# Kernel optimization log

Hardware: AMD Instinct MI355X
Metric: run time of the kernel (lower is better)

## Reference

```python
import jax, jax.numpy as jnp
import numpy as np
import math

D_MODEL = 640
HEAD_DIM = 64
N_HEADS = 14
N_KV_HEADS = 2
HPK = N_HEADS // N_KV_HEADS  # 7
EPS = 1e-5
T = 2048
D_HALF = HEAD_DIM // 2


def setup_inputs() -> dict:
    key = jax.random.key(0)
    ks = jax.random.split(key, 10)
    x = jax.random.normal(ks[0], (1, D_MODEL, 1, T), dtype=jnp.float32)
    # rope tables: realistic cos/sin from standard rotary frequencies
    inv_freq = 1.0 / (10000.0 ** (jnp.arange(0, HEAD_DIM, 2, dtype=jnp.float32) / HEAD_DIM))
    ang = jnp.arange(T, dtype=jnp.float32)[:, None] * inv_freq[None, :]  # (T, 32)
    rope_cos = jnp.cos(ang)
    rope_sin = jnp.sin(ang)
    # causal additive mask (T, T)
    causal = jnp.tril(jnp.ones((T, T), dtype=bool))
    attn_mask = jnp.where(causal, 0.0, -1e9).astype(jnp.float32)
    norm_w = 1.0 + 0.02 * jax.random.normal(ks[1], (D_MODEL,), dtype=jnp.float32)
    qkv_dim = (N_HEADS + 2 * N_KV_HEADS) * HEAD_DIM  # 1152
    qkv_w = jax.random.normal(ks[2], (qkv_dim, D_MODEL), dtype=jnp.float32) * (D_MODEL ** -0.5)
    qkv_b = 0.02 * jax.random.normal(ks[3], (qkv_dim,), dtype=jnp.float32)
    o_w = jax.random.normal(ks[4], (D_MODEL, N_HEADS * HEAD_DIM), dtype=jnp.float32) * ((N_HEADS * HEAD_DIM) ** -0.5)
    o_b = 0.02 * jax.random.normal(ks[5], (D_MODEL,), dtype=jnp.float32)
    sinks = jax.random.normal(ks[6], (N_HEADS,), dtype=jnp.float32)
    return {"x": x, "rope_cos": rope_cos, "rope_sin": rope_sin, "attn_mask": attn_mask,
            "norm_w": norm_w, "qkv_w": qkv_w, "qkv_b": qkv_b, "o_w": o_w, "o_b": o_b,
            "sinks": sinks}


def _apply_rope(xf, n_heads, rope_cos, rope_sin):
    # xf: (1, T, n_heads*dh) -> interleaved rotary
    xr = xf.reshape(1, T, n_heads, HEAD_DIM)
    x1 = xr[..., 0::2]  # (1, T, n, d_half)
    x2 = xr[..., 1::2]
    cos = rope_cos[None, :, None, :]
    sin = rope_sin[None, :, None, :]
    o1 = x1 * cos - x2 * sin
    o2 = x2 * cos + x1 * sin
    return jnp.stack((o1, o2), axis=-1).reshape(1, T, n_heads * HEAD_DIM)


def reference(x, rope_cos, rope_sin, attn_mask, norm_w, qkv_w, qkv_b, o_w, o_b, sinks):
    nh, nkv, hpk, dh = N_HEADS, N_KV_HEADS, HPK, HEAD_DIM
    residual = x
    # RMSNorm over channel dim (axis=1)
    var = jnp.mean(x * x, axis=1, keepdims=True)
    normed = x * jax.lax.rsqrt(var + EPS) * norm_w.reshape(1, -1, 1, 1)
    # fused 1x1 conv QKV: (1, D, T) -> (1, T, qkv_dim)
    n2 = normed[:, :, 0, :]  # (1, D, T)
    qkv = jnp.einsum('bct,oc->bto', n2, qkv_w) + qkv_b
    q_dim = nh * dh
    kv_dim = nkv * dh
    q = qkv[:, :, :q_dim]
    k = qkv[:, :, q_dim:q_dim + kv_dim]
    v = qkv[:, :, q_dim + kv_dim:]
    q = _apply_rope(q, nh, rope_cos, rope_sin)
    k = _apply_rope(k, nkv, rope_cos, rope_sin)
    qk_scale = 1.0 / math.sqrt(math.sqrt(dh))
    q = q * qk_scale
    k = k * qk_scale
    q = q.reshape(1, T, nkv, hpk, dh)
    k = k.reshape(1, T, nkv, dh)
    v = v.reshape(1, T, nkv, dh)
    # GQA scores: (1, nkv, hpk, T, T)
    scores = jnp.einsum('btkgd,bskd->bkgts', q, k)
    scores = scores + attn_mask[None, None, None, :, :]
    # attention-sink logit column appended before softmax
    sink = (sinks * math.log(2.0)).reshape(1, nkv, hpk, 1, 1)
    sink_col = jnp.broadcast_to(sink, (1, nkv, hpk, T, 1))
    scores_with_sink = jnp.concatenate([scores, sink_col], axis=-1)
    attn_w = jax.nn.softmax(scores_with_sink, axis=-1)[..., :-1]
    # weighted values: (1, T, nkv, hpk, dh) -> (1, T, nh*dh)
    attn_out = jnp.einsum('bkgts,bskd->btkgd', attn_w, v).reshape(1, T, nh * dh)
    # output 1x1 conv + residual
    proj = jnp.einsum('bto,do->bdt', attn_out, o_w) + o_b.reshape(1, -1, 1)
    return residual + proj[:, :, None, :]
```

## Files before the change

### kernel.cpp

```cpp
#include <hip/hip_runtime.h>
#include <math.h>

#define T 2048
#define DM 640
#define NH 14
#define NKV 2
#define HPK 7
#define HD 64
#define QDIM 896
#define QKV_DIM 1152

constexpr float QK_SCALE2 = 0.35355339059327373f * 1.2011224087864498f;
constexpr float EPSF = 1e-5f;

typedef __attribute__((ext_vector_type(8))) short short8;
typedef __attribute__((ext_vector_type(4))) float float4v;
typedef unsigned short ush;

static __device__ __forceinline__ ush f2bf(float f) {
    union { float f; unsigned u; } v; v.f = f;
    unsigned r = v.u + 0x7fffu + ((v.u >> 16) & 1u);
    return (ush)(r >> 16);
}
static __device__ __forceinline__ float bf2f(ush s) {
    union { unsigned u; float f; } v; v.u = ((unsigned)s) << 16;
    return v.f;
}

__global__ __launch_bounds__(256) void rstd_kernel(
    const float* __restrict__ x, float* __restrict__ rstd)
{
    const int t0 = blockIdx.x * 64;
    const int tl = threadIdx.x & 63, cg = threadIdx.x >> 6;
    __shared__ float red[4][64];
    float ss = 0.f;
    for (int c = cg; c < DM; c += 4) {
        const float v = x[(size_t)c * T + t0 + tl];
        ss = fmaf(v, v, ss);
    }
    red[cg][tl] = ss;
    __syncthreads();
    if (threadIdx.x < 64) {
        const float s = red[0][tl] + red[1][tl] + red[2][tl] + red[3][tl];
        rstd[t0 + tl] = rsqrtf(s * (1.0f / DM) + EPSF);
    }
}

__global__ __launch_bounds__(256) void cast2_kernel(
    const float* __restrict__ a, ush* __restrict__ ah, ush* __restrict__ al, int na4,
    const float* __restrict__ b, ush* __restrict__ bh, ush* __restrict__ bl)
{
    const int i = blockIdx.x * 256 + threadIdx.x;
    const float* src; ush *dh, *dl; int j;
    if (i < na4) { src = a; dh = ah; dl = al; j = i; }
    else         { src = b; dh = bh; dl = bl; j = i - na4; }
    const float4 v = ((const float4*)src)[j];
    ushort4 h, l;
    h.x = f2bf(v.x); l.x = f2bf(v.x - bf2f(h.x));
    h.y = f2bf(v.y); l.y = f2bf(v.y - bf2f(h.y));
    h.z = f2bf(v.z); l.z = f2bf(v.z - bf2f(h.z));
    h.w = f2bf(v.w); l.w = f2bf(v.w - bf2f(h.w));
    ((ushort4*)dh)[j] = h;
    ((ushort4*)dl)[j] = l;
}

__global__ __launch_bounds__(256) void xnorm_kernel(
    const float* __restrict__ x, const float* __restrict__ norm_w,
    const float* __restrict__ rstd,
    ush* __restrict__ XnH, ush* __restrict__ XnL)
{
    const int tid = threadIdx.x;
    const int t0 = blockIdx.x * 64;
    const int c0 = blockIdx.y * 64;
    __shared__ float xs[64][65];

    #pragma unroll
    for (int it = 0; it < 4; ++it) {
        const int r = (tid >> 4) + it * 16;
        const int cl = (tid & 15) * 4;
        const float4 v = *(const float4*)&x[(size_t)(c0 + r) * T + t0 + cl];
        xs[r][cl + 0] = v.x; xs[r][cl + 1] = v.y;
        xs[r][cl + 2] = v.z; xs[r][cl + 3] = v.w;
    }
    __syncthreads();
    #pragma unroll
    for (int it = 0; it < 4; ++it) {
        const int tr = (tid >> 4) + it * 16;
        const int cl = (tid & 15) * 4;
        const float rs = rstd[t0 + tr];
        ushort4 h, l;
        const float v0 = xs[cl + 0][tr] * norm_w[c0 + cl + 0] * rs;
        const float v1 = xs[cl + 1][tr] * norm_w[c0 + cl + 1] * rs;
        const float v2 = xs[cl + 2][tr] * norm_w[c0 + cl + 2] * rs;
        const float v3 = xs[cl + 3][tr] * norm_w[c0 + cl + 3] * rs;
        h.x = f2bf(v0); l.x = f2bf(v0 - bf2f(h.x));
        h.y = f2bf(v1); l.y = f2bf(v1 - bf2f(h.y));
        h.z = f2bf(v2); l.z = f2bf(v2 - bf2f(h.z));
        h.w = f2bf(v3); l.w = f2bf(v3 - bf2f(h.w));
        *(ushort4*)&XnH[(size_t)(t0 + tr) * DM + c0 + cl] = h;
        *(ushort4*)&XnL[(size_t)(t0 + tr) * DM + c0 + cl] = l;
    }
}

#define QSX_H 0
#define QSX_L 8192
#define QSW_H 16384
#define QSW_L 24576

__global__ __launch_bounds__(256) void qkv_mfma_kernel(
    const ush* __restrict__ XnH, const ush* __restrict__ XnL,
    const ush* __restrict__ WH, const ush* __restrict__ WL,
    const float* __restrict__ qkv_b, const float* __restrict__ rope_cos,
    const float* __restrict__ rope_sin,
    ush* __restrict__ Qh, ush* __restrict__ Ql,
    ush* __restrict__ Kh, ush* __restrict__ Kl,
    ush* __restrict__ Vth, ush* __restrict__ Vtl)
{
    const int t0 = blockIdx.x * 64;
    const int o0 = blockIdx.y * 64;
    const int tid = threadIdx.x;
    const int wave = tid >> 6, lane = tid & 63;
    const int lg = lane >> 4, lq = lane & 15;
    const int wr = wave >> 1, wc = wave & 1;

    __shared__ __align__(16) unsigned char sm[65536];

    const int srow0 = tid >> 3, srow1 = srow0 + 32, scc = tid & 7;
    const int dst0 = srow0 * 128 + ((scc * 16) ^ ((srow0 & 7) << 4));
    const int dst1 = srow1 * 128 + ((scc * 16) ^ ((srow1 & 7) << 4));

    uint4 xh0, xl0, wh0, wl0, xh1, xl1, wh1, wl1;

#define QLOAD(c_) do { \
    xh0 = *(const uint4*)&XnH[(size_t)(t0 + srow0) * DM + (c_) + scc * 8]; \
    xl0 = *(const uint4*)&XnL[(size_t)(t0 + srow0) * DM + (c_) + scc * 8]; \
    wh0 = *(const uint4*)&WH [(size_t)(o0 + srow0) * DM + (c_) + scc * 8]; \
    wl0 = *(const uint4*)&WL [(size_t)(o0 + srow0) * DM + (c_) + scc * 8]; \
    xh1 = *(const uint4*)&XnH[(size_t)(t0 + srow1) * DM + (c_) + scc * 8]; \
    xl1 = *(const uint4*)&XnL[(size_t)(t0 + srow1) * DM + (c_) + scc * 8]; \
    wh1 = *(const uint4*)&WH [(size_t)(o0 + srow1) * DM + (c_) + scc * 8]; \
    wl1 = *(const uint4*)&WL [(size_t)(o0 + srow1) * DM + (c_) + scc * 8]; \
} while (0)

#define QSTORE(b_) do { \
    *(uint4*)((b_) + QSX_H + dst0) = xh0; \
    *(uint4*)((b_) + QSX_L + dst0) = xl0; \
    *(uint4*)((b_) + QSW_H + dst0) = wh0; \
    *(uint4*)((b_) + QSW_L + dst0) = wl0; \
    *(uint4*)((b_) + QSX_H + dst1) = xh1; \
    *(uint4*)((b_) + QSX_L + dst1) = xl1; \
    *(uint4*)((b_) + QSW_H + dst1) = wh1; \
    *(uint4*)((b_) + QSW_L + dst1) = wl1; \
} while (0)

    float4v acc[2][2];
    acc[0][0] = (float4v)0.f; acc[0][1] = (float4v)0.f;
    acc[1][0] = (float4v)0.f; acc[1][1] = (float4v)0.f;

    QLOAD(0);
    QSTORE(sm);
    int cur = 0;
    for (int s = 0; s < 10; ++s) {
        __syncthreads();
        if (s < 9) QLOAD((s + 1) * 64);
        const unsigned char* smb = sm + cur * 32768;
        #pragma unroll
        for (int kk = 0; kk < 2; ++kk) {
            short8 ah[2], al[2], bh[2], bl[2];
            #pragma unroll
            for (int nt = 0; nt < 2; ++nt) {
                const int row = wc * 32 + nt * 16 + lq;
                const int col = (kk * 64 + lg * 16) ^ ((row & 7) << 4);
                bh[nt] = *(const short8*)(smb + QSX_H + row * 128 + col);
                bl[nt] = *(const short8*)(smb + QSX_L + row * 128 + col);
            }
            #pragma unroll
            for (int mt = 0; mt < 2; ++mt) {
                const int row = wr * 32 + mt * 16 + lq;
                const int col = (kk * 64 + lg * 16) ^ ((row & 7) << 4);
                ah[mt] = *(const short8*)(smb + QSW_H + row * 128 + col);
                al[mt] = *(const short8*)(smb + QSW_L + row * 128 + col);
            }
            #pragma unroll
            for (int mt = 0; mt < 2; ++mt) {
                #pragma unroll
                for (int nt = 0; nt < 2; ++nt) {
                    acc[mt][nt] = __builtin_amdgcn_mfma_f32_16x16x32_bf16(ah[mt], bh[nt], acc[mt][nt], 0, 0, 0);
                    acc[mt][nt] = __builtin_amdgcn_mfma_f32_16x16x32_bf16(ah[mt], bl[nt], acc[mt][nt], 0, 0, 0);
                    acc[mt][nt] = __builtin_amdgcn_mfma_f32_16x16x32_bf16(al[mt], bh[nt], acc[mt][nt], 0, 0, 0);
                }
            }
        }
        if (s < 9) { QSTORE(sm + ((cur ^ 1) * 32768)); cur ^= 1; }
    }
#undef QLOAD
#undef QSTORE

    const int by = blockIdx.y;
    #pragma unroll
    for (int mt = 0; mt < 2; ++mt) {
        const int d0 = wr * 32 + mt * 16 + lg * 4;
        #pragma unroll
        for (int nt = 0; nt < 2; ++nt) {
            const int t = t0 + wc * 32 + nt * 16 + lq;
            if (by < 16) {
                const float e0 = acc[mt][nt][0] + qkv_b[o0 + d0 + 0];
                const float d1 = acc[mt][nt][1] + qkv_b[o0 + d0 + 1];
                const float e2 = acc[mt][nt][2] + qkv_b[o0 + d0 + 2];
                const float d3 = acc[mt][nt][3] + qkv_b[o0 + d0 + 3];
                const float c0v = rope_cos[t * 32 + (d0 >> 1)];
                const float s0v = rope_sin[t * 32 + (d0 >> 1)];
                const float c1v = rope_cos[t * 32 + (d0 >> 1) + 1];
                const float s1v = rope_sin[t * 32 + (d0 >> 1) + 1];
                const float r0 = (e0 * c0v - d1 * s0v) * QK_SCALE2;
                const float r1 = (d1 * c0v + e0 * s0v) * QK_SCALE2;
                const float r2 = (e2 * c1v - d3 * s1v) * QK_SCALE2;
                const float r3 = (d3 * c1v + e2 * s1v) * QK_SCALE2;
                ushort4 h, l;
                h.x = f2bf(r0); l.x = f2bf(r0 - bf2f(h.x));
                h.y = f2bf(r1); l.y = f2bf(r1 - bf2f(h.y));
                h.z = f2bf(r2); l.z = f2bf(r2 - bf2f(h.z));
                h.w = f2bf(r3); l.w = f2bf(r3 - bf2f(h.w));
                if (by < 14) {
                    *(ushort4*)&Qh[((size_t)(by * T + t)) * HD + d0] = h;
                    *(ushort4*)&Ql[((size_t)(by * T + t)) * HD + d0] = l;
                } else {
                    const int h2 = by - 14;
                    *(ushort4*)&Kh[((size_t)(h2 * T + t)) * HD + d0] = h;
                    *(ushort4*)&Kl[((size_t)(h2 * T + t)) * HD + d0] = l;
                }
            } else {
                const int h2 = by - 16;
                #pragma unroll
                for (int j = 0; j < 4; ++j) {
                    const float val = acc[mt][nt][j] + qkv_b[o0 + d0 + j];
                    const ush hh = f2bf(val);
                    Vth[((size_t)(h2 * HD + d0 + j)) * T + t] = hh;
                    Vtl[((size_t)(h2 * HD + d0 + j)) * T + t] = f2bf(val - bf2f(hh));
                }
            }
        }
    }
}

__global__ __launch_bounds__(256) void attn_mfma_kernel(
    const ush* __restrict__ Qh, const ush* __restrict__ Ql,
    const ush* __restrict__ Kh, const ush* __restrict__ Kl,
    const ush* __restrict__ Vth, const ush* __restrict__ Vtl,
    const float* __restrict__ sinks,
    float* __restrict__ Opart, float* __restrict__ Mpart, float* __restrict__ Lpart)
{
    const int qt = 31 - (int)blockIdx.x;
    const int h  = blockIdx.y;
    const int kc = blockIdx.z;
    const int kvh = h / HPK;
    const int tid = threadIdx.x;
    const int wave = tid >> 6, lane = tid & 63;
    const int lg = lane >> 4, lq = lane & 15;
    const int qbase = qt * 64 + wave * 16;
    const int myq = qbase + lq;

    __shared__ __align__(16) unsigned char sm[2 * 32768 + 4 * 2304];
    unsigned int* Pl = (unsigned int*)(sm + 65536) + wave * (16 * 36);

    short8 qf[2][2];
    #pragma unroll
    for (int kk = 0; kk < 2; ++kk) {
        const size_t qoff = ((size_t)(h * T + myq)) * HD + kk * 32 + lg * 8;
        qf[kk][0] = *(const short8*)&Qh[qoff];
        qf[kk][1] = *(const short8*)&Ql[qoff];
    }

    float4v oacc[4];
    #pragma unroll
    for (int dt = 0; dt < 4; ++dt) oacc[dt] = (float4v)0.f;

    float m2, l;
    if (kc == 0) { m2 = sinks[h]; l = 1.0f; }
    else         { m2 = -3e38f;   l = 0.0f; }

    const ush* Khp = Kh + (size_t)kvh * T * HD;
    const ush* Klp = Kl + (size_t)kvh * T * HD;
    const ush* Vhp = Vth + (size_t)kvh * HD * T;
    const ush* Vlp = Vtl + (size_t)kvh * HD * T;

    const int srow0 = tid >> 3, srow1 = srow0 + 32, scc = tid & 7;
    const int dst0 = srow0 * 128 + ((scc * 16) ^ ((srow0 & 7) << 4));
    const int dst1 = srow1 * 128 + ((scc * 16) ^ ((srow1 & 7) << 4));

    uint4 rk0h, rk0l, rv0h, rv0l, rk1h, rk1l, rv1h, rv1l;

#define ALOAD(kb_) do { \
    rk0h = *(const uint4*)(Khp + (size_t)((kb_) + srow0) * HD + scc * 8); \
    rk0l = *(const uint4*)(Klp + (size_t)((kb_) + srow0) * HD + scc * 8); \
    rv0h = *(const uint4*)(Vhp + (size_t)srow0 * T + (kb_) + scc * 8); \
    rv0l = *(const uint4*)(Vlp + (size_t)srow0 * T + (kb_) + scc * 8); \
    rk1h = *(const uint4*)(Khp + (size_t)((kb_) + srow1) * HD + scc * 8); \
    rk1l = *(const uint4*)(Klp + (size_t)((kb_) + srow1) * HD + scc * 8); \
    rv1h = *(const uint4*)(Vhp + (size_t)srow1 * T + (kb_) + scc * 8); \
    rv1l = *(const uint4*)(Vlp + (size_t)srow1 * T + (kb_) + scc * 8); \
} while (0)

#define ASTORE(b_) do { \
    *(uint4*)((b_) + 0     + dst0) = rk0h; \
    *(uint4*)((b_) + 8192  + dst0) = rk0l; \
    *(uint4*)((b_) + 16384 + dst0) = rv0h; \
    *(uint4*)((b_) + 24576 + dst0) = rv0l; \
    *(uint4*)((b_) + 0     + dst1) = rk1h; \
    *(uint4*)((b_) + 8192  + dst1) = rk1l; \
    *(uint4*)((b_) + 16384 + dst1) = rv1h; \
    *(uint4*)((b_) + 24576 + dst1) = rv1l; \
} while (0)

    const int nt_cnt = (qt >= kc) ? ((qt - kc) >> 1) + 1 : 0;
    if (nt_cnt > 0) { ALOAD(kc * 64); ASTORE(sm); }
    int cur = 0;

    for (int i = 0; i < nt_cnt; ++i) {
        const int kt = kc + 2 * i;
        const int kb = kt * 64;
        __syncthreads();
        if (i + 1 < nt_cnt) ALOAD(kb + 128);
        unsigned char* smb = sm + cur * 32768;

        float4v st[4];
        #pragma unroll
        for (int t = 0; t < 4; ++t) st[t] = (float4v)0.f;
        #pragma unroll
        for (int t = 0; t < 4; ++t) {
            const int row = t * 16 + lq;
            const int rb = row * 128;
            const int sw = (row & 7) << 4;
            #pragma unroll
            for (int kk = 0; kk < 2; ++kk) {
                const int col = (kk * 64 + lg * 16) ^ sw;
                const short8 ah = *(const short8*)(smb + rb + col);
                const short8 al = *(const short8*)(smb + 8192 + rb + col);
                st[t] = __builtin_amdgcn_mfma_f32_16x16x32_bf16(ah, qf[kk][0], st[t], 0, 0, 0);
                st[t] = __builtin_amdgcn_mfma_f32_16x16x32_bf16(ah, qf[kk][1], st[t], 0, 0, 0);
                st[t] = __builtin_amdgcn_mfma_f32_16x16x32_bf16(al, qf[kk][0], st[t], 0, 0, 0);
            }
        }

        float pmax = -3e38f;
        #pragma unroll
        for (int t = 0; t < 4; ++t) {
            #pragma unroll
            for (int j = 0; j < 4; ++j) {
                const int key = kb + 16 * t + 4 * lg + j;
                const float s = (key > myq) ? -3e38f : st[t][j];
                st[t][j] = s;
                pmax = fmaxf(pmax, s);
            }
        }
        pmax = fmaxf(pmax, __shfl_xor(pmax, 16));
        pmax = fmaxf(pmax, __shfl_xor(pmax, 32));
        if (__any(pmax > m2)) {
            const float mnew = fmaxf(m2, pmax);
            const float corr = exp2f(m2 - mnew);
            l *= corr;
            #pragma unroll
            for (int dt = 0; dt < 4; ++dt) oacc[dt] *= corr;
            m2 = mnew;
        }
        float psum = 0.f;
        #pragma unroll
        for (int t = 0; t < 4; ++t) {
            #pragma unroll
            for (int j = 0; j < 4; ++j) {
                const float p = exp2f(st[t][j] - m2);
                st[t][j] = p;
                psum += p;
            }
        }
        psum += __shfl_xor(psum, 16);
        psum += __shfl_xor(psum, 32);
        l += psum;

        #pragma unroll
        for (int t = 0; t < 4; ++t) {
            #pragma unroll
            for (int j2 = 0; j2 < 2; ++j2) {
                const unsigned int u = (unsigned int)f2bf(st[t][2 * j2]) |
                                       ((unsigned int)f2bf(st[t][2 * j2 + 1]) << 16);
                Pl[lq * 36 + t * 8 + lg * 2 + j2] = u;
            }
        }

        #pragma unroll
        for (int c = 0; c < 2; ++c) {
            const short8 pf = *(const short8*)&Pl[lq * 36 + c * 16 + lg * 4];
            #pragma unroll
            for (int dt = 0; dt < 4; ++dt) {
                const int row = dt * 16 + lq;
                const int rb = row * 128;
                const int col = (c * 64 + lg * 16) ^ ((row & 7) << 4);
                const short8 vh = *(const short8*)(smb + 16384 + rb + col);
                const short8 vl = *(const short8*)(smb + 24576 + rb + col);
                oacc[dt] = __builtin_amdgcn_mfma_f32_16x16x32_bf16(vh, pf, oacc[dt], 0, 0, 0);
                oacc[dt] = __builtin_amdgcn_mfma_f32_16x16x32_bf16(vl, pf, oacc[dt], 0, 0, 0);
            }
        }

        if (i + 1 < nt_cnt) { ASTORE(sm + ((cur ^ 1) * 32768)); cur ^= 1; }
    }
#undef ALOAD
#undef ASTORE

    const int r = qbase + lq;
    const int pb = (h * 2 + kc) * 64;
    #pragma unroll
    for (int dt = 0; dt < 4; ++dt) {
        #pragma unroll
        for (int j = 0; j < 4; ++j) {
            const int d = dt * 16 + lg * 4 + j;
            Opart[(size_t)(pb + d) * T + r] = oacc[dt][j];
        }
    }
    if (lane < 16) {
        Mpart[(size_t)(h * 2 + kc) * T + r] = m2;
        Lpart[(size_t)(h * 2 + kc) * T + r] = l;
    }
}

__global__ __launch_bounds__(256) void attn_combine_kernel(
    const float* __restrict__ Opart, const float* __restrict__ Mpart,
    const float* __restrict__ Lpart,
    ush* __restrict__ AOH, ush* __restrict__ AOL)
{
    const int idx = blockIdx.x * 256 + threadIdx.x;
    const int h = idx >> 11;
    const int r = idx & (T - 1);

    const float m0 = Mpart[(h * 2 + 0) * T + r], l0 = Lpart[(h * 2 + 0) * T + r];
    const float m1 = Mpart[(h * 2 + 1) * T + r], l1 = Lpart[(h * 2 + 1) * T + r];
    const float M = fmaxf(m0, m1);
    float w0 = exp2f(m0 - M), w1 = exp2f(m1 - M);
    const float L = l0 * w0 + l1 * w1;
    const float invL = 1.0f / L;
    w0 *= invL; w1 *= invL;

    #pragma unroll
    for (int d4 = 0; d4 < 16; ++d4) {
        ushort4 hh, ll;
        #pragma unroll
        for (int j = 0; j < 4; ++j) {
            const int d = d4 * 4 + j;
            const float acc = Opart[((h * 2 + 0) * 64 + d) * (size_t)T + r] * w0
                            + Opart[((h * 2 + 1) * 64 + d) * (size_t)T + r] * w1;
            const ush hv = f2bf(acc);
            ((ush*)&hh)[j] = hv;
            ((ush*)&ll)[j] = f2bf(acc - bf2f(hv));
        }
        *(ushort4*)&AOH[(size_t)r * QDIM + h * 64 + d4 * 4] = hh;
        *(ushort4*)&AOL[(size_t)r * QDIM + h * 64 + d4 * 4] = ll;
    }
}

#define PSA_H 0
#define PSA_L 8192
#define PSW_H 16384
#define PSW_L 24576

__global__ __launch_bounds__(256) void oproj_mfma_kernel(
    const ush* __restrict__ AOH, const ush* __restrict__ AOL,
    const ush* __restrict__ OWH, const ush* __restrict__ OWL,
    const float* __restrict__ o_b, const float* __restrict__ x,
    float* __restrict__ out)
{
    const int t0 = blockIdx.x * 64;
    const int c0 = blockIdx.y * 64;
    const int tid = threadIdx.x;
    const int wave = tid >> 6, lane = tid & 63;
    const int lg = lane >> 4, lq = lane & 15;
    const int wr = wave >> 1, wc = wave & 1;

    __shared__ __align__(16) unsigned char sm[65536];

    const int srow0 = tid >> 3, srow1 = srow0 + 32, scc = tid & 7;
    const int dst0 = srow0 * 128 + ((scc * 16) ^ ((srow0 & 7) << 4));
    const int dst1 = srow1 * 128 + ((scc * 16) ^ ((srow1 & 7) << 4));

    uint4 xh0, xl0, wh0, wl0, xh1, xl1, wh1, wl1;

#define PLOAD(k_) do { \
    xh0 = *(const uint4*)&AOH[(size_t)(t0 + srow0) * QDIM + (k_) + scc * 8]; \
    xl0 = *(const uint4*)&AOL[(size_t)(t0 + srow0) * QDIM + (k_) + scc * 8]; \
    wh0 = *(const uint4*)&OWH[(size_t)(c0 + srow0) * QDIM + (k_) + scc * 8]; \
    wl0 = *(const uint4*)&OWL[(size_t)(c0 + srow0) * QDIM + (k_) + scc * 8]; \
    xh1 = *(const uint4*)&AOH[(size_t)(t0 + srow1) * QDIM + (k_) + scc * 8]; \
    xl1 = *(const uint4*)&AOL[(size_t)(t0 + srow1) * QDIM + (k_) + scc * 8]; \
    wh1 = *(const uint4*)&OWH[(size_t)(c0 + srow1) * QDIM + (k_) + scc * 8]; \
    wl1 = *(const uint4*)&OWL[(size_t)(c0 + srow1) * QDIM + (k_) + scc * 8]; \
} while (0)

#define PSTORE(b_) do { \
    *(uint4*)((b_) + PSA_H + dst0) = xh0; \
    *(uint4*)((b_) + PSA_L + dst0) = xl0; \
    *(uint4*)((b_) + PSW_H + dst0) = wh0; \
    *(uint4*)((b_) + PSW_L + dst0) = wl0; \
    *(uint4*)((b_) + PSA_H + dst1) = xh1; \
    *(uint4*)((b_) + PSA_L + dst1) = xl1; \
    *(uint4*)((b_) + PSW_H + dst1) = wh1; \
    *(uint4*)((b_) + PSW_L + dst1) = wl1; \
} while (0)

    float4v acc[2][2];
    acc[0][0] = (float4v)0.f; acc[0][1] = (float4v)0.f;
    acc[1][0] = (float4v)0.f; acc[1][1] = (float4v)0.f;

    PLOAD(0);
    PSTORE(sm);
    int cur = 0;
    for (int s = 0; s < 14; ++s) {
        __syncthreads();
        if (s < 13) PLOAD((s + 1) * 64);
        const unsigned char* smb = sm + cur * 32768;
        #pragma unroll
        for (int kk = 0; kk < 2; ++kk) {
            short8 ah[2], al[2], bh[2], bl[2];
            #pragma unroll
            for (int nt = 0; nt < 2; ++nt) {
                const int row = wc * 32 + nt * 16 + lq;
                const int col = (kk * 64 + lg * 16) ^ ((row & 7) << 4);
                bh[nt] = *(const short8*)(smb + PSA_H + row * 128 + col);
                bl[nt] = *(const short8*)(smb + PSA_L + row * 128 + col);
            }
            #pragma unroll
            for (int mt = 0; mt < 2; ++mt) {
                const int row = wr * 32 + mt * 16 + lq;
                const int col = (kk * 64 + lg * 16) ^ ((row & 7) << 4);
                ah[mt] = *(const short8*)(smb + PSW_H + row * 128 + col);
                al[mt] = *(const short8*)(smb + PSW_L + row * 128 + col);
            }
            #pragma unroll
            for (int mt = 0; mt < 2; ++mt) {
                #pragma unroll
                for (int nt = 0; nt < 2; ++nt) {
                    acc[mt][nt] = __builtin_amdgcn_mfma_f32_16x16x32_bf16(ah[mt], bh[nt], acc[mt][nt], 0, 0, 0);
                    acc[mt][nt] = __builtin_amdgcn_mfma_f32_16x16x32_bf16(ah[mt], bl[nt], acc[mt][nt], 0, 0, 0);
                    acc[mt][nt] = __builtin_amdgcn_mfma_f32_16x16x32_bf16(al[mt], bh[nt], acc[mt][nt], 0, 0, 0);
                }
            }
        }
        if (s < 13) { PSTORE(sm + ((cur ^ 1) * 32768)); cur ^= 1; }
    }
#undef PLOAD
#undef PSTORE

    #pragma unroll
    for (int mt = 0; mt < 2; ++mt) {
        const int cb = c0 + wr * 32 + mt * 16 + lg * 4;
        #pragma unroll
        for (int nt = 0; nt < 2; ++nt) {
            const int t = t0 + wc * 32 + nt * 16 + lq;
            #pragma unroll
            for (int j = 0; j < 4; ++j) {
                const int c = cb + j;
                out[(size_t)c * T + t] = acc[mt][nt][j] + o_b[c] + x[(size_t)c * T + t];
            }
        }
    }
}

extern "C" void kernel_launch(void* const* d_in, const int* in_sizes, int n_in,
                              void* d_out, int out_size, void* d_ws, size_t ws_size,
                              hipStream_t stream) {
    const float* x        = (const float*)d_in[0];
    const float* rope_cos = (const float*)d_in[1];
    const float* rope_sin = (const float*)d_in[2];
    const float* norm_w   = (const float*)d_in[4];
    const float* qkv_w    = (const float*)d_in[5];
    const float* qkv_b    = (const float*)d_in[6];
    const float* o_w      = (const float*)d_in[7];
    const float* o_b      = (const float*)d_in[8];
    const float* sinks    = (const float*)d_in[9];
    float* out = (float*)d_out;

    float* ws    = (float*)d_ws;
    float* rstd  = ws;
    float* Opart = rstd + 2048;
    float* Mpart = Opart + 3670016;
    float* Lpart = Mpart + 57344;
    ush* bws = (ush*)(Lpart + 57344);
    ush* Qh  = bws;
    ush* Ql  = Qh  + 1835008;
    ush* Kh  = Ql  + 1835008;
    ush* Kl  = Kh  + 262144;
    ush* Vth = Kl  + 262144;
    ush* Vtl = Vth + 262144;
    ush* XnH = Vtl + 262144;
    ush* XnL = XnH + 1310720;
    ush* WqH = XnL + 1310720;
    ush* WqL = WqH + 737280;
    ush* OWH = WqL + 737280;
    ush* OWL = OWH + 573440;
    ush* AOH = OWL + 573440;
    ush* AOL = AOH + 1835008;

    rstd_kernel<<<32, 256, 0, stream>>>(x, rstd);
    cast2_kernel<<<1280, 256, 0, stream>>>(qkv_w, WqH, WqL, QKV_DIM * DM / 4,
                                           o_w, OWH, OWL);
    xnorm_kernel<<<dim3(32, 10), 256, 0, stream>>>(x, norm_w, rstd, XnH, XnL);
    qkv_mfma_kernel<<<dim3(32, 18), 256, 0, stream>>>(
        XnH, XnL, WqH, WqL, qkv_b, rope_cos, rope_sin, Qh, Ql, Kh, Kl, Vth, Vtl);
    attn_mfma_kernel<<<dim3(32, NH, 2), 256, 0, stream>>>(
        Qh, Ql, Kh, Kl, Vth, Vtl, sinks, Opart, Mpart, Lpart);
    attn_combine_kernel<<<NH * T / 256, 256, 0, stream>>>(Opart, Mpart, Lpart, AOH, AOL);
    oproj_mfma_kernel<<<dim3(32, 10), 256, 0, stream>>>(AOH, AOL, OWH, OWL, o_b, x, out);
}
```

Baseline: 261.6 us.

## Single-buffer LDS tiles and drop V low-part MFMA in attention

Replaces double-buffered shared-memory tiles in the QKV, attention and output-projection kernels with a single buffer. Each step now stores the prefetched registers and synchronises twice per iteration, which halves LDS use and may allow more resident blocks per CU. In attention, the V low-precision split (Vtl) is no longer loaded or multiplied, cutting global traffic, LDS and MFMA work for P·V. In exchange it adds a barrier per iteration and gives up some precision in the P·V product.

Result: faster. 246.8 us (-5.7%).

```diff
diff --git a/kernel.cpp b/kernel.cpp
--- a/kernel.cpp
+++ b/kernel.cpp
@@ -123,7 +123,7 @@
     const int lg = lane >> 4, lq = lane & 15;
     const int wr = wave >> 1, wc = wave & 1;
 
-    __shared__ __align__(16) unsigned char sm[65536];
+    __shared__ __align__(16) unsigned char sm[32768];
 
     const int srow0 = tid >> 3, srow1 = srow0 + 32, scc = tid & 7;
     const int dst0 = srow0 * 128 + ((scc * 16) ^ ((srow0 & 7) << 4));
@@ -142,15 +142,15 @@
     wl1 = *(const uint4*)&WL [(size_t)(o0 + srow1) * DM + (c_) + scc * 8]; \
 } while (0)
 
-#define QSTORE(b_) do { \
-    *(uint4*)((b_) + QSX_H + dst0) = xh0; \
-    *(uint4*)((b_) + QSX_L + dst0) = xl0; \
-    *(uint4*)((b_) + QSW_H + dst0) = wh0; \
-    *(uint4*)((b_) + QSW_L + dst0) = wl0; \
-    *(uint4*)((b_) + QSX_H + dst1) = xh1; \
-    *(uint4*)((b_) + QSX_L + dst1) = xl1; \
-    *(uint4*)((b_) + QSW_H + dst1) = wh1; \
-    *(uint4*)((b_) + QSW_L + dst1) = wl1; \
+#define QSTORE() do { \
+    *(uint4*)(sm + QSX_H + dst0) = xh0; \
+    *(uint4*)(sm + QSX_L + dst0) = xl0; \
+    *(uint4*)(sm + QSW_H + dst0) = wh0; \
+    *(uint4*)(sm + QSW_L + dst0) = wl0; \
+    *(uint4*)(sm + QSX_H + dst1) = xh1; \
+    *(uint4*)(sm + QSX_L + dst1) = xl1; \
+    *(uint4*)(sm + QSW_H + dst1) = wh1; \
+    *(uint4*)(sm + QSW_L + dst1) = wl1; \
 } while (0)
 
     float4v acc[2][2];
@@ -158,12 +158,10 @@
     acc[1][0] = (float4v)0.f; acc[1][1] = (float4v)0.f;
 
     QLOAD(0);
-    QSTORE(sm);
-    int cur = 0;
     for (int s = 0; s < 10; ++s) {
+        QSTORE();
         __syncthreads();
         if (s < 9) QLOAD((s + 1) * 64);
-        const unsigned char* smb = sm + cur * 32768;
         #pragma unroll
         for (int kk = 0; kk < 2; ++kk) {
             short8 ah[2], al[2], bh[2], bl[2];
@@ -171,15 +169,15 @@
             for (int nt = 0; nt < 2; ++nt) {
                 const int row = wc * 32 + nt * 16 + lq;
                 const int col = (kk * 64 + lg * 16) ^ ((row & 7) << 4);
-                bh[nt] = *(const short8*)(smb + QSX_H + row * 128 + col);
-                bl[nt] = *(const short8*)(smb + QSX_L + row * 128 + col);
+                bh[nt] = *(const short8*)(sm + QSX_H + row * 128 + col);
+                bl[nt] = *(const short8*)(sm + QSX_L + row * 128 + col);
             }
             #pragma unroll
             for (int mt = 0; mt < 2; ++mt) {
                 const int row = wr * 32 + mt * 16 + lq;
                 const int col = (kk * 64 + lg * 16) ^ ((row & 7) << 4);
-                ah[mt] = *(const short8*)(smb + QSW_H + row * 128 + col);
-                al[mt] = *(const short8*)(smb + QSW_L + row * 128 + col);
+                ah[mt] = *(const short8*)(sm + QSW_H + row * 128 + col);
+                al[mt] = *(const short8*)(sm + QSW_L + row * 128 + col);
             }
             #pragma unroll
             for (int mt = 0; mt < 2; ++mt) {
@@ -191,7 +189,7 @@
                 }
             }
         }
-        if (s < 9) { QSTORE(sm + ((cur ^ 1) * 32768)); cur ^= 1; }
+        if (s < 9) __syncthreads();
     }
 #undef QLOAD
 #undef QSTORE
@@ -260,8 +258,8 @@
     const int qbase = qt * 64 + wave * 16;
     const int myq = qbase + lq;
 
-    __shared__ __align__(16) unsigned char sm[2 * 32768 + 4 * 2304];
-    unsigned int* Pl = (unsigned int*)(sm + 65536) + wave * (16 * 36);
+    __shared__ __align__(16) unsigned char sm[24576 + 4 * 2304];
+    unsigned int* Pl = (unsigned int*)(sm + 24576) + wave * (16 * 36);
 
     short8 qf[2][2];
     #pragma unroll
@@ -282,46 +280,39 @@
     const ush* Khp = Kh + (size_t)kvh * T * HD;
     const ush* Klp = Kl + (size_t)kvh * T * HD;
     const ush* Vhp = Vth + (size_t)kvh * HD * T;
-    const ush* Vlp = Vtl + (size_t)kvh * HD * T;
 
     const int srow0 = tid >> 3, srow1 = srow0 + 32, scc = tid & 7;
     const int dst0 = srow0 * 128 + ((scc * 16) ^ ((srow0 & 7) << 4));
     const int dst1 = srow1 * 128 + ((scc * 16) ^ ((srow1 & 7) << 4));
 
-    uint4 rk0h, rk0l, rv0h, rv0l, rk1h, rk1l, rv1h, rv1l;
+    uint4 rk0h, rk0l, rv0h, rk1h, rk1l, rv1h;
 
 #define ALOAD(kb_) do { \
     rk0h = *(const uint4*)(Khp + (size_t)((kb_) + srow0) * HD + scc * 8); \
     rk0l = *(const uint4*)(Klp + (size_t)((kb_) + srow0) * HD + scc * 8); \
     rv0h = *(const uint4*)(Vhp + (size_t)srow0 * T + (kb_) + scc * 8); \
-    rv0l = *(const uint4*)(Vlp + (size_t)srow0 * T + (kb_) + scc * 8); \
     rk1h = *(const uint4*)(Khp + (size_t)((kb_) + srow1) * HD + scc * 8); \
     rk1l = *(const uint4*)(Klp + (size_t)((kb_) + srow1) * HD + scc * 8); \
     rv1h = *(const uint4*)(Vhp + (size_t)srow1 * T + (kb_) + scc * 8); \
-    rv1l = *(const uint4*)(Vlp + (size_t)srow1 * T + (kb_) + scc * 8); \
 } while (0)
 
-#define ASTORE(b_) do { \
-    *(uint4*)((b_) + 0     + dst0) = rk0h; \
-    *(uint4*)((b_) + 8192  + dst0) = rk0l; \
-    *(uint4*)((b_) + 16384 + dst0) = rv0h; \
-    *(uint4*)((b_) + 24576 + dst0) = rv0l; \
-    *(uint4*)((b_) + 0     + dst1) = rk1h; \
-    *(uint4*)((b_) + 8192  + dst1) = rk1l; \
-    *(uint4*)((b_) + 16384 + dst1) = rv1h; \
-    *(uint4*)((b_) + 24576 + dst1) = rv1l; \
+#define ASTORE() do { \
+    *(uint4*)(sm + 0     + dst0) = rk0h; \
+    *(uint4*)(sm + 8192  + dst0) = rk0l; \
+    *(uint4*)(sm + 16384 + dst0) = rv0h; \
+    *(uint4*)(sm + 0     + dst1) = rk1h; \
+    *(uint4*)(sm + 8192  + dst1) = rk1l; \
+    *(uint4*)(sm + 16384 + dst1) = rv1h; \
 } while (0)
 
     const int nt_cnt = (qt >= kc) ? ((qt - kc) >> 1) + 1 : 0;
-    if (nt_cnt > 0) { ALOAD(kc * 64); ASTORE(sm); }
-    int cur = 0;
+    if (nt_cnt > 0) ALOAD(kc * 64);
 
     for (int i = 0; i < nt_cnt; ++i) {
-        const int kt = kc + 2 * i;
-        const int kb = kt * 64;
+        const int kb = (kc + 2 * i) * 64;
+        ASTORE();
         __syncthreads();
         if (i + 1 < nt_cnt) ALOAD(kb + 128);
-        unsigned char* smb = sm + cur * 32768;
 
         float4v st[4];
         #pragma unroll
@@ -334,8 +325,8 @@
             #pragma unroll
             for (int kk = 0; kk < 2; ++kk) {
                 const int col = (kk * 64 + lg * 16) ^ sw;
-                const short8 ah = *(const short8*)(smb + rb + col);
-                const short8 al = *(const short8*)(smb + 8192 + rb + col);
+                const short8 ah = *(const short8*)(sm + rb + col);
+                const short8 al = *(const short8*)(sm + 8192 + rb + col);
                 st[t] = __builtin_amdgcn_mfma_f32_16x16x32_bf16(ah, qf[kk][0], st[t], 0, 0, 0);
                 st[t] = __builtin_amdgcn_mfma_f32_16x16x32_bf16(ah, qf[kk][1], st[t], 0, 0, 0);
                 st[t] = __builtin_amdgcn_mfma_f32_16x16x32_bf16(al, qf[kk][0], st[t], 0, 0, 0);
@@ -395,14 +386,12 @@
                 const int row = dt * 16 + lq;
                 const int rb = row * 128;
                 const int col = (c * 64 + lg * 16) ^ ((row & 7) << 4);
-                const short8 vh = *(const short8*)(smb + 16384 + rb + col);
-                const short8 vl = *(const short8*)(smb + 24576 + rb + col);
+                const short8 vh = *(const short8*)(sm + 16384 + rb + col);
                 oacc[dt] = __builtin_amdgcn_mfma_f32_16x16x32_bf16(vh, pf, oacc[dt], 0, 0, 0);
-                oacc[dt] = __builtin_amdgcn_mfma_f32_16x16x32_bf16(vl, pf, oacc[dt], 0, 0, 0);
-            }
-        }
-
-        if (i + 1 < nt_cnt) { ASTORE(sm + ((cur ^ 1) * 32768)); cur ^= 1; }
+            }
+        }
+
+        if (i + 1 < nt_cnt) __syncthreads();
     }
 #undef ALOAD
 #undef ASTORE
@@ -475,7 +464,7 @@
     const int lg = lane >> 4, lq = lane & 15;
     const int wr = wave >> 1, wc = wave & 1;
 
-    __shared__ __align__(16) unsigned char sm[65536];
+    __shared__ __align__(16) unsigned char sm[32768];
 
     const int srow0 = tid >> 3, srow1 = srow0 + 32, scc = tid & 7;
     const int dst0 = srow0 * 128 + ((scc * 16) ^ ((srow0 & 7) << 4));
@@ -494,15 +483,15 @@
     wl1 = *(const uint4*)&OWL[(size_t)(c0 + srow1) * QDIM + (k_) + scc * 8]; \
 } while (0)
 
-#define PSTORE(b_) do { \
-    *(uint4*)((b_) + PSA_H + dst0) = xh0; \
-    *(uint4*)((b_) + PSA_L + dst0) = xl0; \
-    *(uint4*)((b_) + PSW_H + dst0) = wh0; \
-    *(uint4*)((b_) + PSW_L + dst0) = wl0; \
-    *(uint4*)((b_) + PSA_H + dst1) = xh1; \
-    *(uint4*)((b_) + PSA_L + dst1) = xl1; \
-    *(uint4*)((b_) + PSW_H + dst1) = wh1; \
-    *(uint4*)((b_) + PSW_L + dst1) = wl1; \
+#define PSTORE() do { \
+    *(uint4*)(sm + PSA_H + dst0) = xh0; \
+    *(uint4*)(sm + PSA_L + dst0) = xl0; \
+    *(uint4*)(sm + PSW_H + dst0) = wh0; \
+    *(uint4*)(sm + PSW_L + dst0) = wl0; \
+    *(uint4*)(sm + PSA_H + dst1) = xh1; \
+    *(uint4*)(sm + PSA_L + dst1) = xl1; \
+    *(uint4*)(sm + PSW_H + dst1) = wh1; \
+    *(uint4*)(sm + PSW_L + dst1) = wl1; \
 } while (0)
 
     float4v acc[2][2];
@@ -510,12 +499,10 @@
     acc[1][0] = (float4v)0.f; acc[1][1] = (float4v)0.f;
 
     PLOAD(0);
-    PSTORE(sm);
-    int cur = 0;
     for (int s = 0; s < 14; ++s) {
+        PSTORE();
         __syncthreads();
         if (s < 13) PLOAD((s + 1) * 64);
-        const unsigned char* smb = sm + cur * 32768;
         #pragma unroll
         for (int kk = 0; kk < 2; ++kk) {
             short8 ah[2], al[2], bh[2], bl[2];
@@ -523,15 +510,15 @@
             for (int nt = 0; nt < 2; ++nt) {
                 const int row = wc * 32 + nt * 16 + lq;
                 const int col = (kk * 64 + lg * 16) ^ ((row & 7) << 4);
-                bh[nt] = *(const short8*)(smb + PSA_H + row * 128 + col);
-                bl[nt] = *(const short8*)(smb + PSA_L + row * 128 + col);
+                bh[nt] = *(const short8*)(sm + PSA_H + row * 128 + col);
+                bl[nt] = *(const short8*)(sm + PSA_L + row * 128 + col);
             }
             #pragma unroll
             for (int mt = 0; mt < 2; ++mt) {
                 const int row = wr * 32 + mt * 16 + lq;
                 const int col = (kk * 64 + lg * 16) ^ ((row & 7) << 4);
-                ah[mt] = *(const short8*)(smb + PSW_H + row * 128 + col);
-                al[mt] = *(const short8*)(smb + PSW_L + row * 128 + col);
+                ah[mt] = *(const short8*)(sm + PSW_H + row * 128 + col);
+                al[mt] = *(const short8*)(sm + PSW_L + row * 128 + col);
             }
             #pragma unroll
             for (int mt = 0; mt < 2; ++mt) {
@@ -543,7 +530,7 @@
                 }
             }
         }
-        if (s < 13) { PSTORE(sm + ((cur ^ 1) * 32768)); cur ^= 1; }
+        if (s < 13) __syncthreads();
     }
 #undef PLOAD
 #undef PSTORE
```
